# Optimization experiments

Hardware: AMD Instinct MI355X
Metric: run time of the kernel (lower is better)

The kernel has to match this reference:

```python
import jax, jax.numpy as jnp
import numpy as np
from jax import lax

BATCH = 32; SEQ_LEN = 336; ENC_IN = 7; MARK_IN = 4
D_MODEL = 512; D_FF = 2048; N_HEADS = 8; DK = 64; DV = 64
E_LAYERS = 3; D_BOTTLE = 128; PRED_LEN = 96
WINDOW = (4, 4, 4); INNER = 5


def _mask_sizes():
    # Pyraformer get_mask: True = masked out
    all_size = [SEQ_LEN]
    for w in WINDOW:
        all_size.append(all_size[-1] // w)
    S = sum(all_size)
    m = np.zeros((S, S), bool)  # True = may attend
    iw = INNER // 2
    starts = np.cumsum([0] + all_size)
    for l, sz in enumerate(all_size):
        st = int(starts[l])
        for i in range(st, st + sz):
            m[i, max(i - iw, st):min(i + iw + 1, st + sz)] = True
    for l in range(1, len(all_size)):
        st = int(starts[l])
        for i in range(st, st + all_size[l]):
            left = (st - all_size[l - 1]) + (i - st) * WINDOW[l - 1]
            right = st if i == st + all_size[l] - 1 else (st - all_size[l - 1]) + (i - st + 1) * WINDOW[l - 1]
            m[i, left:right] = True
            m[left:right, i] = True
    return ~m, all_size


def _refer_points(all_size):
    idx = np.zeros((all_size[0], len(all_size)), np.int64)
    for i in range(all_size[0]):
        idx[i, 0] = i
        former = i
        for j in range(1, len(all_size)):
            start = sum(all_size[:j])
            inner = former - (start - all_size[j - 1])
            former = start + min(inner // WINDOW[j - 1], all_size[j] - 1)
            idx[i, j] = former
    return idx


def _pos_enc(L, d):
    pos = np.arange(L)[:, None].astype(np.float32)
    div = np.exp(np.arange(0, d, 2).astype(np.float32) * (-np.log(10000.0) / d))
    pe = np.zeros((L, d), np.float32)
    pe[:, 0::2] = np.sin(pos * div)
    pe[:, 1::2] = np.cos(pos * div)
    return pe


def _ln(x, g, b, eps=1e-5):
    mu = jnp.mean(x, -1, keepdims=True)
    v = jnp.mean((x - mu) ** 2, -1, keepdims=True)
    return (x - mu) * lax.rsqrt(v + eps) * g + b


def setup_inputs():
    key = jax.random.key(0)
    ks = iter(jax.random.split(key, 64))
    def nrm(shape, s=0.02):
        return jax.random.normal(next(ks), shape, jnp.float32) * s
    mask, all_size = _mask_sizes()
    inp = {
        "x_enc": jax.random.normal(next(ks), (BATCH, SEQ_LEN, ENC_IN), jnp.float32),
        "x_mark_enc": jax.random.normal(next(ks), (BATCH, SEQ_LEN, MARK_IN), jnp.float32),
        "x_dec": jax.random.normal(next(ks), (BATCH, PRED_LEN, ENC_IN), jnp.float32),
        "x_mark_dec": jax.random.normal(next(ks), (BATCH, PRED_LEN, MARK_IN), jnp.float32),
        "conv_embed_w": nrm((D_MODEL, ENC_IN, 3), 0.1),
        "time_w": nrm((MARK_IN, D_MODEL)),
        "time_b": jnp.zeros((D_MODEL,), jnp.float32),
        "down_w": nrm((D_MODEL, D_BOTTLE)),
        "down_b": jnp.zeros((D_BOTTLE,), jnp.float32),
        "cscm_conv_w": nrm((3, D_BOTTLE, D_BOTTLE, 4), 0.05),
        "cscm_conv_b": jnp.zeros((3, D_BOTTLE), jnp.float32),
        "bn_g": jnp.ones((3, D_BOTTLE), jnp.float32),
        "bn_b": jnp.zeros((3, D_BOTTLE), jnp.float32),
        "up_w": nrm((D_BOTTLE, D_MODEL)),
        "up_b": jnp.zeros((D_MODEL,), jnp.float32),
        "cscm_ln_g": jnp.ones((D_MODEL,), jnp.float32),
        "cscm_ln_b": jnp.zeros((D_MODEL,), jnp.float32),
        "wq": nrm((E_LAYERS, D_MODEL, N_HEADS * DK)),
        "wk": nrm((E_LAYERS, D_MODEL, N_HEADS * DK)),
        "wv": nrm((E_LAYERS, D_MODEL, N_HEADS * DV)),
        "wo": nrm((E_LAYERS, N_HEADS * DV, D_MODEL)),
        "ln1_g": jnp.ones((E_LAYERS, D_MODEL), jnp.float32),
        "ln1_b": jnp.zeros((E_LAYERS, D_MODEL), jnp.float32),
        "ffn_w1": nrm((E_LAYERS, D_MODEL, D_FF)),
        "ffn_b1": jnp.zeros((E_LAYERS, D_FF), jnp.float32),
        "ffn_w2": nrm((E_LAYERS, D_FF, D_MODEL)),
        "ffn_b2": jnp.zeros((E_LAYERS, D_MODEL), jnp.float32),
        "ln2_g": jnp.ones((E_LAYERS, D_MODEL), jnp.float32),
        "ln2_b": jnp.zeros((E_LAYERS, D_MODEL), jnp.float32),
        "pred_w": nrm((len(all_size) * D_MODEL, PRED_LEN * ENC_IN)),
        "attn_mask": jnp.asarray(mask),                 # [S,S] bool, True = masked
        "indexes": jnp.asarray(_refer_points(all_size)),  # [336, 4] int64
    }
    return inp


def _forward(x_enc, x_mark_enc, conv_embed_w, time_w, time_b, down_w, down_b,
             cscm_conv_w, cscm_conv_b, bn_g, bn_b, up_w, up_b, cscm_ln_g, cscm_ln_b,
             wq, wk, wv, wo, ln1_g, ln1_b, ffn_w1, ffn_b1, ffn_w2, ffn_b2, ln2_g, ln2_b,
             pred_w, attn_mask, indexes):
    B = x_enc.shape[0]
    dn = ('NWC', 'OIW', 'NWC')
    # DataEmbedding: circular conv1d token embedding + sinusoidal pos + linear time-feature embedding
    xp = jnp.concatenate([x_enc[:, -1:], x_enc, x_enc[:, :1]], axis=1)  # circular pad, k=3
    tok = lax.conv_general_dilated(xp, conv_embed_w, (1,), 'VALID', dimension_numbers=dn)
    pe = jnp.asarray(_pos_enc(SEQ_LEN, D_MODEL))
    emb = tok + pe[None] + x_mark_enc @ time_w + time_b  # [B,336,512]
    # Bottleneck_Construct (CSCM): down-proj, strided convs per scale, up-proj, concat, LN
    x = emb @ down_w + down_b  # [B,336,128]
    outs = []
    for i in range(len(WINDOW)):
        x = lax.conv_general_dilated(x, cscm_conv_w[i], (WINDOW[i],), 'VALID', dimension_numbers=dn) + cscm_conv_b[i]
        x = x * bn_g[i] + bn_b[i]  # eval-mode BatchNorm1d (running mean 0 / var 1)
        x = jax.nn.elu(x)
        outs.append(x)  # lengths 84, 21, 5
    coarse = jnp.concatenate(outs, axis=1) @ up_w + up_b  # [B,110,512]
    seq = _ln(jnp.concatenate([emb, coarse], axis=1), cscm_ln_g, cscm_ln_b)  # [B,446,512]
    S = seq.shape[1]
    neg = jnp.where(attn_mask, jnp.float32(-1e9), jnp.float32(0.0))  # [S,S]
    scale = 1.0 / np.sqrt(DK).astype(np.float32)
    for l in range(E_LAYERS):  # post-norm encoder layers
        q = (seq @ wq[l]).reshape(B, S, N_HEADS, DK)
        k = (seq @ wk[l]).reshape(B, S, N_HEADS, DK)
        v = (seq @ wv[l]).reshape(B, S, N_HEADS, DV)
        attn = jax.nn.softmax(jnp.einsum('bihd,bjhd->bhij', q, k) * scale + neg, axis=-1)
        o = jnp.einsum('bhij,bjhd->bihd', attn, v).reshape(B, S, N_HEADS * DV)
        seq = _ln(seq + o @ wo[l], ln1_g[l], ln1_b[l])
        h = jax.nn.gelu(seq @ ffn_w1[l] + ffn_b1[l], approximate=False)
        seq = _ln(seq + h @ ffn_w2[l] + ffn_b2[l], ln2_g[l], ln2_b[l])
    # pyramidal readout: gather each scale's ancestor node for every fine position
    g = seq[:, indexes.reshape(-1), :].reshape(B, SEQ_LEN, -1)  # [B,336,4*512]
    enc_out = g[:, -1, :]  # [B,2048]
    return (enc_out @ pred_w).reshape(B, PRED_LEN, ENC_IN)


def reference(x_enc, x_mark_enc, x_dec, x_mark_dec, conv_embed_w, time_w, time_b,
              down_w, down_b, cscm_conv_w, cscm_conv_b, bn_g, bn_b, up_w, up_b,
              cscm_ln_g, cscm_ln_b, wq, wk, wv, wo, ln1_g, ln1_b, ffn_w1, ffn_b1,
              ffn_w2, ffn_b2, ln2_g, ln2_b, pred_w, attn_mask, indexes):
    # x_dec / x_mark_dec are unused by Pyraformer's forward (kept for signature parity)
    return _forward(x_enc, x_mark_enc, conv_embed_w, time_w, time_b, down_w, down_b,
                    cscm_conv_w, cscm_conv_b, bn_g, bn_b, up_w, up_b, cscm_ln_g, cscm_ln_b,
                    wq, wk, wv, wo, ln1_g, ln1_b, ffn_w1, ffn_b1, ffn_w2, ffn_b2,
                    ln2_g, ln2_b, pred_w, attn_mask, indexes)
```

## Files before the change

kernel.cpp:

```cpp
#include <hip/hip_runtime.h>
#include <math.h>

constexpr int BB   = 32;
constexpr int L    = 336;
constexpr int CIN  = 7;
constexpr int MARK = 4;
constexpr int D    = 512;
constexpr int DFF  = 2048;
constexpr int NH   = 8;
constexpr int HD   = 64;
constexpr int S    = 446;
constexpr int DBOT = 128;
constexpr int L1 = 84, L2 = 21, L3 = 5;
constexpr int LC = 110;
constexpr int NLAYER = 3;
constexpr int PRED_N = 672;
constexpr int MP   = 14336;
constexpr int NMAX = 12;
constexpr int MCONV1 = BB * L1;
constexpr int MCONV2P = 768;
constexpr int MCAT  = 3584;

using short8  = __attribute__((ext_vector_type(8))) short;
using float4v = __attribute__((ext_vector_type(4))) float;

struct SetsData {
    int nbr[S][NMAX];
    int idx[4][S];
    int cnt[4];
};

constexpr SetsData compute_sets() {
    SetsData sd{};
    constexpr int sizes[4]  = {336, 84, 21, 5};
    constexpr int starts[4] = {0, 336, 420, 441};
    for (int i = 0; i < S; ++i) {
        int li = 0, pi = i;
        if (i < 336)      { li = 0; pi = i; }
        else if (i < 420) { li = 1; pi = i - 336; }
        else if (i < 441) { li = 2; pi = i - 420; }
        else              { li = 3; pi = i - 441; }
        int cnt = 0;
        for (int d = -2; d <= 2; ++d) {
// ... 36 lines not shown

constexpr size_t psk_elems() {
    size_t mx = 4 * (size_t)BB * L * DBOT;
    {
        size_t v = 4 * (size_t)MCONV1 * DBOT; if (v > mx) mx = v;
        v = 4 * (size_t)MCONV2P * DBOT;       if (v > mx) mx = v;
    }
    for (int l = 0; l < NLAYER; ++l) {
        size_t Mc = (size_t)HS.cnt[l + 1] * 32;
        size_t Mpad = ((Mc + 127) / 128) * 128;
        { size_t v = 4 * Mpad * 512;  if (v > mx) mx = v; }
        if (Mc <= 512) { size_t v = 4 * Mpad * 2048; if (v > mx) mx = v; }
        size_t ks = (Mc <= 512) ? 8 : 4;
        size_t v = ks * Mpad * 512; if (v > mx) mx = v;
    }
    return mx;
}

__device__ inline short f2bf(float f) {
    union { float f; unsigned u; } v; v.f = f;
    unsigned r = v.u + 0x7fffu + ((v.u >> 16) & 1u);
    return (short)(r >> 16);
}
__device__ inline float bf2f(short h) {
    union { unsigned u; float f; } v; v.u = ((unsigned)(unsigned short)h) << 16;
    return v.f;
}

__device__ inline void gload_lds16(const void* g, void* l) {
    __builtin_amdgcn_global_load_lds(
        (const __attribute__((address_space(1))) void*)g,
        (__attribute__((address_space(3))) void*)l, 16, 0, 0);
}


template<int EPI>
__launch_bounds__(256, 4)
__global__ void mfma_gemm(const short* __restrict__ A, const short* __restrict__ Bt,
                          const float* __restrict__ bias, const float* __restrict__ bias2,
                          void* __restrict__ Cout, int Kd, int Nd,
                          int alvl, int clvl, int cnt,
                          const float* __restrict__ peT, short* __restrict__ Cout2) {
    __shared__ short As[2][128 * 32];
    __shared__ short Bs[2][128 * 32];
    int tid = threadIdx.x;
    int nwg  = gridDim.x * gridDim.y;
    int orig = blockIdx.y * gridDim.x + blockIdx.x;
    int qq = nwg >> 3, rr = nwg & 7;
    int xcd = orig & 7, idx = orig >> 3;
    int wgid = (xcd < rr ? xcd * (qq + 1) : rr * (qq + 1) + (xcd - rr) * qq) + idx;
    int m0 = (wgid / gridDim.x) * 128, n0 = (wgid % gridDim.x) * 128;

    int lane = tid & 63, wid = tid >> 6;
    int wm = wid >> 1, wn = wid & 1;
    int lr = lane & 15, lk = lane >> 4;

    size_t abase[2], bbase[2];
#pragma unroll
    for (int r = 0; r < 2; ++r) {
        int u = r * 256 + tid;
        int row = ((u >> 3) << 1) | ((u >> 2) & 1);
        int kg  = (u & 3) ^ ((u >> 3) & 3);
        int rm = m0 + row, ga;
        if (alvl >= 0) { int j = rm >> 5; if (j > cnt - 1) j = cnt - 1; ga = (rm & 31) * S + d_sets.idx[alvl][j]; }
        else ga = rm;
        abase[r] = (size_t)ga * Kd + kg * 8;
// ... 266 lines not shown
        __builtin_amdgcn_s_barrier();
    }

#pragma unroll
    for (int mi = 0; mi < 4; ++mi) {
        int gmc = m0 + wm * 64 + mi * 16 + lk * 4;
#pragma unroll
        for (int ni = 0; ni < 4; ++ni) {
            int gn = n0 + wn * 64 + ni * 16 + lr;
#pragma unroll
            for (int e = 0; e < 4; ++e)
                part[((size_t)kz * Mpad + gmc + e) * Nd + gn] = acc[mi][ni][e];
        }
    }
}

template<int EPI>
__launch_bounds__(256)
__global__ void reduce_sk(const float* __restrict__ part, const float* __restrict__ bias,
                          const float* __restrict__ bias2, short* __restrict__ Cout,
                          int Mpad, int Nd, int KS) {
    int idx = blockIdx.x * 256 + threadIdx.x;
    if (idx >= Mpad * Nd) return;
    float s = 0.0f;
    for (int k = 0; k < KS; ++k)
        s += part[(size_t)k * Mpad * Nd + idx];
    int n = idx % Nd;
    if (EPI == 3 || EPI == 4) s += bias[n];
    if (EPI == 3) s = 0.5f * s * (1.0f + erff(s * 0.70710678118654752f));
    if (EPI == 5) { s = s * bias[n] + bias2[n]; s = s > 0.0f ? s : (expf(s) - 1.0f); }
    Cout[idx] = f2bf(s);
}

__device__ inline void wtrans_tile(const float* __restrict__ W, short* __restrict__ Wt,
                                   int Kd, int Nd, int n0, int k0, int tid) {
    __shared__ float tile[32][33];
    int tx = tid & 31, ty = tid >> 5;
#pragma unroll
    for (int r = 0; r < 32; r += 8)
        tile[ty + r][tx] = W[(size_t)(k0 + ty + r) * Nd + n0 + tx];
    __syncthreads();
#pragma unroll
    for (int r = 0; r < 32; r += 8)
        Wt[(size_t)(n0 + ty + r) * Kd + k0 + tx] = f2bf(tile[tx][ty + r]);
}

constexpr int PE_N  = L * D;
constexpr int WE_N  = D * 32;
constexpr int XIM_N = BB * L * 32;
constexpr int MISC_N = PE_N + WE_N + XIM_N;
constexpr int PREP_BLKS = 3072 + 6144 + 640 + (MISC_N + 255) / 256;

__launch_bounds__(256)
__global__ void prep_all(const float* __restrict__ wq, const float* __restrict__ wk,
                         const float* __restrict__ wv, const float* __restrict__ wo,
                         short* __restrict__ wqkvT, short* __restrict__ woT,
                         const float* __restrict__ w1, const float* __restrict__ w2,
                         short* __restrict__ w1T, short* __restrict__ w2T,
                         const float* __restrict__ down_w, short* __restrict__ downT,
                         const float* __restrict__ up_w, short* __restrict__ upT,
                         const float* __restrict__ cw, const float* __restrict__ cb,
                         const float* __restrict__ bg, const float* __restrict__ bb,
                         short* __restrict__ cscmT, float* __restrict__ sc,
                         float* __restrict__ sh,
                         const float* __restrict__ x_enc, const float* __restrict__ x_mark,
                         const float* __restrict__ cew, const float* __restrict__ tw,
                         const float* __restrict__ tb, float* __restrict__ pe,
                         short* __restrict__ wE, short* __restrict__ xim) {
    int blk = blockIdx.x;
    int tid = threadIdx.x;
    if (blk < 3072) {
        int z = blk >> 8, rem = blk & 255;
        int l = z >> 2, part = z & 3;
        const float* src = (part == 0 ? wq : part == 1 ? wk : part == 2 ? wv : wo)
                           + (size_t)l * D * D;
        short* dst = (part < 3) ? wqkvT + (size_t)l * 3 * D * D + (size_t)part * D * D
                                : woT + (size_t)l * D * D;
        wtrans_tile(src, dst, D, D, (rem & 15) * 32, (rem >> 4) * 32, tid);
        return;
    }
    blk -= 3072;
    if (blk < 6144) {
        int z = blk >> 10, rem = blk & 1023;
        int l = z >> 1, part = z & 1;
        int bx = rem & 63, by = rem >> 6;
        int nt = part ? by : bx;
        int kt = part ? bx : by;
        if (part == 0)
            wtrans_tile(w1 + (size_t)l * D * DFF, w1T + (size_t)l * DFF * D,
                        D, DFF, nt * 32, kt * 32, tid);
        else
            wtrans_tile(w2 + (size_t)l * DFF * D, w2T + (size_t)l * D * DFF,
                        DFF, D, nt * 32, kt * 32, tid);
        return;
    }
    blk -= 6144;
    if (blk < 640) {
        if (blk < 64) {
            wtrans_tile(down_w, downT, D, DBOT, (blk & 3) * 32, (blk >> 2) * 32, tid);
        } else if (blk < 128) {
            int b2 = blk - 64;
            wtrans_tile(up_w, upT, DBOT, D, (b2 & 15) * 32, (b2 >> 4) * 32, tid);
        } else {
            int idx = (blk - 128) * 256 + tid;
            if (idx < 2 * DBOT * 512) {
                int l = idx >> 16;
                int rem = idx & 65535;
                int oc = rem >> 9, j = rem & 511;
                int r = j >> 7, c = j & 127;
                cscmT[idx] = f2bf(cw[(((size_t)l * DBOT + oc) * DBOT + c) * 4 + r]);
            }
            if (idx < 3 * DBOT) {
                sc[idx] = bg[idx];
                sh[idx] = cb[idx] * bg[idx] + bb[idx];
            }
        }
        return;
    }
    blk -= 640;
    {
        int idx = blk * 256 + tid;
        if (idx < PE_N) {
            int d = idx % D, t = idx / D;
            int e = d & ~1;
            float div = expf(-(float)e * (logf(10000.0f) / (float)D));
            float arg = (float)t * div;
            pe[idx] = (d & 1) ? cosf(arg) : sinf(arg);
            return;
        }
        int i2 = idx - PE_N;
        if (i2 < WE_N) {
            int k = i2 & 31, d = i2 >> 5;
            float v = 0.0f;
            if (k < 21) {
                int w = k / 7, i = k % 7;
// ... 70 lines not shown
#pragma unroll
    for (int jj = 0; jj < NMAX; ++jj) {
        float s = -1e30f;
        if (nb[jj] >= 0) {
            const short8 kv = *(const short8*)(QKV + (size_t)(b * S + nb[jj]) * 1536 + 512 + lane * 8);
            s = 0.0f;
#pragma unroll
            for (int e = 0; e < 8; ++e) s += qf[e] * bf2f(kv[e]);
            s += __shfl_xor(s, 1); s += __shfl_xor(s, 2); s += __shfl_xor(s, 4);
            s *= 0.125f;
        }
        sc[jj] = s;
    }
    float mx = sc[0];
#pragma unroll
    for (int jj = 1; jj < NMAX; ++jj) mx = fmaxf(mx, sc[jj]);
    float sum = 0.0f;
    float accv[8] = {};
#pragma unroll
    for (int jj = 0; jj < NMAX; ++jj) {
        float p = expf(sc[jj] - mx);
        sum += p;
        if (nb[jj] >= 0) {
            const short8 vv = *(const short8*)(QKV + (size_t)(b * S + nb[jj]) * 1536 + 1024 + lane * 8);
#pragma unroll
            for (int e = 0; e < 8; ++e) accv[e] += p * bf2f(vv[e]);
        }
    }
    float inv = 1.0f / sum;
    short8 ov;
#pragma unroll
    for (int e = 0; e < 8; ++e) ov[e] = f2bf(accv[e] * inv);
    *(short8*)(Ob + (size_t)wid * D + lane * 8) = ov;
}

__device__ inline float blk_reduce(float v, float* ws4, int tid) {
#pragma unroll
    for (int o = 32; o; o >>= 1) v += __shfl_xor(v, o);
    if ((tid & 63) == 0) ws4[tid >> 6] = v;
    __syncthreads();
    return ws4[0] + ws4[1] + ws4[2] + ws4[3];
}

__launch_bounds__(256)
__global__ void concat_ln_idx(const short* __restrict__ emb_bf, const float* __restrict__ coarse,
                              const float* __restrict__ g, const float* __restrict__ bta,
                              float* __restrict__ seq, short* __restrict__ seq_bf) {
    int row = blockIdx.x;
    int b = row & 31, j = row >> 5;
    int s = d_sets.idx[0][j];
    int orig = b * S + s;
    __shared__ float wsA[4];
    __shared__ float wsB[4];
    int tid = threadIdx.x;
    float x0, x1;
    if (s < L) {
        const short* src = emb_bf + ((size_t)b * L + s) * D;
        x0 = bf2f(src[tid]); x1 = bf2f(src[tid + 256]);
    } else {
        const float* src = coarse + ((size_t)b * LC + (s - L)) * D;
        x0 = src[tid]; x1 = src[tid + 256];
    }
    float mu = blk_reduce(x0 + x1, wsA, tid) * (1.0f / D);
    float d0 = x0 - mu, d1 = x1 - mu;
    float var = blk_reduce(d0 * d0 + d1 * d1, wsB, tid) * (1.0f / D);
    float rstd = rsqrtf(var + 1e-5f);
    float v0 = d0 * rstd * g[tid]       + bta[tid];
    float v1 = d1 * rstd * g[tid + 256] + bta[tid + 256];
    float* dst = seq + (size_t)orig * D;
    dst[tid] = v0; dst[tid + 256] = v1;
    short* dbf = seq_bf + (size_t)orig * D;
    dbf[tid] = f2bf(v0); dbf[tid + 256] = f2bf(v1);
}

// ... 34 lines not shown
                            float* __restrict__ part) {
    __shared__ float es[32][257];
    __shared__ float wsm[256][8];
    int tid = threadIdx.x;
    int n0 = blockIdx.x * 8;
    int ks = blockIdx.y;
    int k0 = ks * 256;
    const int pos[4] = {335, 419, 440, 445};
    int seg = ks >> 1;
    int dbase = (ks & 1) * 256;
#pragma unroll 8
    for (int r = 0; r < 32; ++r)
        es[r][tid] = seq[((size_t)r * S + pos[seg]) * D + dbase + tid];
#pragma unroll
    for (int e = 0; e < 8; ++e)
        wsm[tid][e] = w[(size_t)(k0 + tid) * PRED_N + n0 + e];
    __syncthreads();
    int b = tid >> 3, nn = tid & 7;
    float acc = 0.0f;
#pragma unroll 8
    for (int kk = 0; kk < 256; ++kk)
        acc += es[b][kk] * wsm[kk][nn];
    part[(size_t)ks * (BB * PRED_N) + (size_t)b * PRED_N + n0 + nn] = acc;
}

__launch_bounds__(256)
__global__ void pred_reduce_kernel(const float* __restrict__ part, float* __restrict__ out) {
    int idx = blockIdx.x * 256 + threadIdx.x;
    if (idx >= BB * PRED_N) return;
    float s = 0.0f;
#pragma unroll
    for (int k = 0; k < 8; ++k) s += part[(size_t)k * (BB * PRED_N) + idx];
    out[idx] = s;
}

extern "C" void kernel_launch(void* const* d_in, const int* in_sizes, int n_in,
                              void* d_out, int out_size, void* d_ws, size_t ws_size,
                              hipStream_t stream) {
    const float* x_enc      = (const float*)d_in[0];
    const float* x_mark_enc = (const float*)d_in[1];
    const float* conv_embed_w = (const float*)d_in[4];
    const float* time_w  = (const float*)d_in[5];
    const float* time_b  = (const float*)d_in[6];
    const float* down_w  = (const float*)d_in[7];
    const float* down_b  = (const float*)d_in[8];
    const float* cscm_w  = (const float*)d_in[9];
    const float* cscm_b  = (const float*)d_in[10];
    const float* bn_g    = (const float*)d_in[11];
    const float* bn_b    = (const float*)d_in[12];
    const float* up_w    = (const float*)d_in[13];
    const float* up_b    = (const float*)d_in[14];
    const float* cln_g   = (const float*)d_in[15];
    const float* cln_b   = (const float*)d_in[16];
    const float* wq      = (const float*)d_in[17];
    const float* wk      = (const float*)d_in[18];
    const float* wv      = (const float*)d_in[19];
    const float* wo      = (const float*)d_in[20];
    const float* ln1_g   = (const float*)d_in[21];
    const float* ln1_b   = (const float*)d_in[22];
    const float* ffn_w1  = (const float*)d_in[23];
    const float* ffn_b1  = (const float*)d_in[24];
    const float* ffn_w2  = (const float*)d_in[25];
    const float* ffn_b2  = (const float*)d_in[26];
    const float* ln2_g   = (const float*)d_in[27];
    const float* ln2_b   = (const float*)d_in[28];
    const float* pred_w  = (const float*)d_in[29];
    float* out = (float*)d_out;

    char* w8 = (char*)d_ws;
    size_t off = 0;
    auto alloc = [&](size_t bytes) {
        void* p = w8 + off;
        off = (off + bytes + 255) & ~(size_t)255;
        return p;
    };
    short* emb_bf = (short*)alloc((size_t)BB * L * D * 2);
    float* pe     = (float*)alloc((size_t)L * D * 4);
    short* xim    = (short*)alloc((size_t)BB * L * 32 * 2);
    short* wE     = (short*)alloc((size_t)D * 32 * 2);
    short* xd_bf  = (short*)alloc((size_t)BB * L * DBOT * 2);
    short* cs1_bf = (short*)alloc((size_t)MCONV2P * 512 * 2);
    short* cs2_bf = (short*)alloc((size_t)MCONV2P * DBOT * 2);
    short* cs3_bf = (short*)alloc((size_t)BB * L3 * DBOT * 2);
    float* coarse = (float*)alloc((size_t)MCAT * D * 4);
    float* seq    = (float*)alloc((size_t)BB * S * D * 4);
    float* part   = (float*)alloc((size_t)8 * BB * PRED_N * 4);
    float* partsk = (float*)alloc(psk_elems() * 4);
    short* seq_bf = (short*)alloc((size_t)MP * D * 2);
    short* QKV    = (short*)alloc((size_t)MP * 3 * D * 2);
    short* Ob     = (short*)alloc((size_t)MP * D * 2);
    short* hidden = QKV;
    short* wqkvT  = (short*)alloc((size_t)NLAYER * 3 * D * D * 2);
    short* woT    = (short*)alloc((size_t)NLAYER * D * D * 2);
    short* w1T    = (short*)alloc((size_t)NLAYER * DFF * D * 2);
    short* w2T    = (short*)alloc((size_t)NLAYER * D * DFF * 2);
    short* downT  = (short*)alloc((size_t)DBOT * D * 2);
    short* upT    = (short*)alloc((size_t)D * DBOT * 2);
    short* cscmT  = (short*)alloc((size_t)2 * DBOT * 512 * 2);
    float* csc_sc = (float*)alloc((size_t)3 * DBOT * 4);
    float* csc_sh = (float*)alloc((size_t)3 * DBOT * 4);
    (void)ws_size; (void)in_sizes; (void)n_in; (void)out_size;

    const int rowsL = BB * L;
    dim3 blk(256);

    prep_all<<<dim3(PREP_BLKS), blk, 0, stream>>>(
        wq, wk, wv, wo, wqkvT, woT,
        ffn_w1, ffn_w2, w1T, w2T,
        down_w, downT, up_w, upT,
        cscm_w, cscm_b, bn_g, bn_b, cscmT, csc_sc, csc_sh,
        x_enc, x_mark_enc, conv_embed_w, time_w, time_b, pe, wE, xim);
    mfma_gemm<6><<<dim3(D / 128, rowsL / 128), blk, 0, stream>>>(
        xim, wE, nullptr, nullptr, nullptr, 32, D, -1, -1, 0, pe, emb_bf);
    mfma_gemm_sk<<<dim3(1, rowsL / 128, 4), blk, 0, stream>>>(
        emb_bf, downT, partsk, D, DBOT, -1, 0);
    reduce_sk<4><<<dim3((rowsL * DBOT + 255) / 256), blk, 0, stream>>>(
        partsk, down_b, nullptr, xd_bf, rowsL, DBOT, 4);
    mfma_gemm_sk<<<dim3(1, MCONV1 / 128, 4), blk, 0, stream>>>(
        xd_bf, cscmT, partsk, 512, DBOT, -1, 0);
    reduce_sk<5><<<dim3((MCONV1 * DBOT + 255) / 256), blk, 0, stream>>>(
        partsk, csc_sc, csc_sh, cs1_bf, MCONV1, DBOT, 4);
    mfma_gemm_sk<<<dim3(1, MCONV2P / 128, 4), blk, 0, stream>>>(
        cs1_bf, cscmT + (size_t)DBOT * 512, partsk, 512, DBOT, -1, 0);
    reduce_sk<5><<<dim3((MCONV2P * DBOT + 255) / 256), blk, 0, stream>>>(
        partsk, csc_sc + DBOT, csc_sh + DBOT, cs2_bf, MCONV2P, DBOT, 4);
    cscm_conv_bf16<<<dim3(BB * L3), dim3(DBOT), 0, stream>>>(
        cs2_bf, L2, cs3_bf, cscm_w + 2 * DBOT * DBOT * 4,
        cscm_b + 2 * DBOT, bn_g + 2 * DBOT, bn_b + 2 * DBOT, L3);
    mfma_gemm_up<<<dim3(D / 128, MCAT / 128), blk, 0, stream>>>(
        cs1_bf, cs2_bf, cs3_bf, upT, up_b, coarse);
    concat_ln_idx<<<dim3(HS.cnt[0] * 32), blk, 0, stream>>>(
        emb_bf, coarse, cln_g, cln_b, seq, seq_bf);

    for (int l = 0; l < NLAYER; ++l) {
        const int inLvl = l, outLvl = l + 1;
        const int inCnt  = HS.cnt[l];
        const int outCnt = HS.cnt[l + 1];
        const int Mc   = outCnt * 32;
// ... 35 lines not shown
```

Baseline: 328.6 us.

## Fuse entire forward pass into one persistent cooperative kernel with grid syncs

Replaces the chain of separate kernel launches (prep, embedding GEMM, CSCM convs, per-layer QKV/attention/out-proj/FFN, LayerNorms, prediction) with a single persistent cooperative kernel. Stages run as virtual-block loops separated by grid.sync. Split-K reductions are folded into the add+LayerNorm row stages, and down/conv GEMMs now run without split-K. This removes launch overhead and inter-kernel gaps, but every stage boundary becomes a grid-wide barrier and small stages leave most blocks idle. It falls back to the old multi-kernel path if the cooperative launch fails.

Result: slower. 1.193 ms (+262.9%).

```diff
diff --git a/kernel.cpp b/kernel.cpp
--- a/kernel.cpp
+++ b/kernel.cpp
@@ -1,5 +1,8 @@
 #include <hip/hip_runtime.h>
+#include <hip/hip_cooperative_groups.h>
 #include <math.h>
+
+namespace cg = cooperative_groups;
 
 constexpr int BB   = 32;
 constexpr int L    = 336;
@@ -7,8 +10,6 @@
 constexpr int MARK = 4;
 constexpr int D    = 512;
 constexpr int DFF  = 2048;
-constexpr int NH   = 8;
-constexpr int HD   = 64;
 constexpr int S    = 446;
 constexpr int DBOT = 128;
 constexpr int L1 = 84, L2 = 21, L3 = 5;
@@ -111,6 +112,20 @@
         (const __attribute__((address_space(1))) void*)g,
         (__attribute__((address_space(3))) void*)l, 16, 0, 0);
 }
+
+__device__ inline float blk_reduce(float v, float* ws4, int tid) {
+#pragma unroll
+    for (int o = 32; o; o >>= 1) v += __shfl_xor(v, o);
+    if ((tid & 63) == 0) ws4[tid >> 6] = v;
+    __syncthreads();
+    return ws4[0] + ws4[1] + ws4[2] + ws4[3];
+}
+
+constexpr int PE_N  = L * D;
+constexpr int WE_N  = D * 32;
+constexpr int XIM_N = BB * L * 32;
+constexpr int MISC_N = PE_N + WE_N + XIM_N;
+constexpr int PREP_BLKS = 3072 + 6144 + 640 + (MISC_N + 255) / 256;
 
 
 template<int EPI>
@@ -443,8 +458,8 @@
     Cout[idx] = f2bf(s);
 }
 
-__device__ inline void wtrans_tile(const float* __restrict__ W, short* __restrict__ Wt,
-                                   int Kd, int Nd, int n0, int k0, int tid) {
+__device__ inline void wtrans_tile_s(const float* __restrict__ W, short* __restrict__ Wt,
+                                     int Kd, int Nd, int n0, int k0, int tid) {
     __shared__ float tile[32][33];
     int tx = tid & 31, ty = tid >> 5;
 #pragma unroll
@@ -455,12 +470,6 @@
     for (int r = 0; r < 32; r += 8)
         Wt[(size_t)(n0 + ty + r) * Kd + k0 + tx] = f2bf(tile[tx][ty + r]);
 }
-
-constexpr int PE_N  = L * D;
-constexpr int WE_N  = D * 32;
-constexpr int XIM_N = BB * L * 32;
-constexpr int MISC_N = PE_N + WE_N + XIM_N;
-constexpr int PREP_BLKS = 3072 + 6144 + 640 + (MISC_N + 255) / 256;
 
 __launch_bounds__(256)
 __global__ void prep_all(const float* __restrict__ wq, const float* __restrict__ wk,
@@ -487,7 +496,7 @@
                            + (size_t)l * D * D;
         short* dst = (part < 3) ? wqkvT + (size_t)l * 3 * D * D + (size_t)part * D * D
                                 : woT + (size_t)l * D * D;
-        wtrans_tile(src, dst, D, D, (rem & 15) * 32, (rem >> 4) * 32, tid);
+        wtrans_tile_s(src, dst, D, D, (rem & 15) * 32, (rem >> 4) * 32, tid);
         return;
     }
     blk -= 3072;
@@ -498,20 +507,20 @@
         int nt = part ? by : bx;
         int kt = part ? bx : by;
         if (part == 0)
-            wtrans_tile(w1 + (size_t)l * D * DFF, w1T + (size_t)l * DFF * D,
-                        D, DFF, nt * 32, kt * 32, tid);
+            wtrans_tile_s(w1 + (size_t)l * D * DFF, w1T + (size_t)l * DFF * D,
+                          D, DFF, nt * 32, kt * 32, tid);
         else
-            wtrans_tile(w2 + (size_t)l * DFF * D, w2T + (size_t)l * D * DFF,
-                        DFF, D, nt * 32, kt * 32, tid);
+            wtrans_tile_s(w2 + (size_t)l * DFF * D, w2T + (size_t)l * D * DFF,
+                          DFF, D, nt * 32, kt * 32, tid);
         return;
     }
     blk -= 6144;
     if (blk < 640) {
         if (blk < 64) {
-            wtrans_tile(down_w, downT, D, DBOT, (blk & 3) * 32, (blk >> 2) * 32, tid);
+            wtrans_tile_s(down_w, downT, D, DBOT, (blk & 3) * 32, (blk >> 2) * 32, tid);
         } else if (blk < 128) {
             int b2 = blk - 64;
-            wtrans_tile(up_w, upT, DBOT, D, (b2 & 15) * 32, (b2 >> 4) * 32, tid);
+            wtrans_tile_s(up_w, upT, DBOT, D, (b2 & 15) * 32, (b2 >> 4) * 32, tid);
         } else {
             int idx = (blk - 128) * 256 + tid;
             if (idx < 2 * DBOT * 512) {
@@ -648,14 +657,6 @@
 #pragma unroll
     for (int e = 0; e < 8; ++e) ov[e] = f2bf(accv[e] * inv);
     *(short8*)(Ob + (size_t)wid * D + lane * 8) = ov;
-}
-
-__device__ inline float blk_reduce(float v, float* ws4, int tid) {
-#pragma unroll
-    for (int o = 32; o; o >>= 1) v += __shfl_xor(v, o);
-    if ((tid & 63) == 0) ws4[tid >> 6] = v;
-    __syncthreads();
-    return ws4[0] + ws4[1] + ws4[2] + ws4[3];
 }
 
 __launch_bounds__(256)
@@ -756,6 +757,505 @@
 #pragma unroll
     for (int k = 0; k < 8; ++k) s += part[(size_t)k * (BB * PRED_N) + idx];
     out[idx] = s;
+}
+
+
+struct P {
+    const float *x_enc, *x_mark, *cew, *tw, *tb;
+    const float *down_w, *down_b, *cscm_w, *cscm_b, *bn_g, *bn_b;
+    const float *up_w, *up_b, *cln_g, *cln_b;
+    const float *wq, *wk, *wv, *wo, *ln1_g, *ln1_b;
+    const float *w1, *b1, *w2, *b2, *ln2_g, *ln2_b, *pred_w;
+    float* out;
+    short *emb_bf, *xim, *wE, *xd_bf, *cs1, *cs2, *cs3;
+    short *seq_bf, *QKV, *Ob;
+    short *wqkvT, *woT, *w1T, *w2T, *downT, *upT, *cscmT;
+    float *pe, *coarse, *seq, *part, *partsk, *csc_sc, *csc_sh;
+};
+
+__device__ inline void wtrans_tile_p(const float* __restrict__ W, short* __restrict__ Wt,
+                                     int Kd, int Nd, int n0, int k0, int tid,
+                                     float (*tile)[33]) {
+    int tx = tid & 31, ty = tid >> 5;
+#pragma unroll
+    for (int r = 0; r < 32; r += 8)
+        tile[ty + r][tx] = W[(size_t)(k0 + ty + r) * Nd + n0 + tx];
+    __syncthreads();
+#pragma unroll
+    for (int r = 0; r < 32; r += 8)
+        Wt[(size_t)(n0 + ty + r) * Kd + k0 + tx] = f2bf(tile[tx][ty + r]);
+}
+
+__device__ inline void prep_vb(const P& p, int blk, int tid, float (*tile)[33]) {
+    if (blk < 3072) {
+        int z = blk >> 8, rem = blk & 255;
+        int l = z >> 2, part = z & 3;
+        const float* src = (part == 0 ? p.wq : part == 1 ? p.wk : part == 2 ? p.wv : p.wo)
+                           + (size_t)l * D * D;
+        short* dst = (part < 3) ? p.wqkvT + (size_t)l * 3 * D * D + (size_t)part * D * D
+                                : p.woT + (size_t)l * D * D;
+        wtrans_tile_p(src, dst, D, D, (rem & 15) * 32, (rem >> 4) * 32, tid, tile);
+    } else if (blk < 3072 + 6144) {
+        int b2 = blk - 3072;
+        int z = b2 >> 10, rem = b2 & 1023;
+        int l = z >> 1, part = z & 1;
+        int bx = rem & 63, by = rem >> 6;
+        int nt = part ? by : bx;
+        int kt = part ? bx : by;
+        if (part == 0)
+            wtrans_tile_p(p.w1 + (size_t)l * D * DFF, p.w1T + (size_t)l * DFF * D,
+                          D, DFF, nt * 32, kt * 32, tid, tile);
+        else
+            wtrans_tile_p(p.w2 + (size_t)l * DFF * D, p.w2T + (size_t)l * D * DFF,
+                          DFF, D, nt * 32, kt * 32, tid, tile);
+    } else if (blk < 3072 + 6144 + 640) {
+        int b3 = blk - (3072 + 6144);
+        if (b3 < 64) {
+            wtrans_tile_p(p.down_w, p.downT, D, DBOT, (b3 & 3) * 32, (b3 >> 2) * 32, tid, tile);
+        } else if (b3 < 128) {
+            int b4 = b3 - 64;
+            wtrans_tile_p(p.up_w, p.upT, DBOT, D, (b4 & 15) * 32, (b4 >> 4) * 32, tid, tile);
+        } else {
+            int idx = (b3 - 128) * 256 + tid;
+            if (idx < 2 * DBOT * 512) {
+                int l = idx >> 16;
+                int rem = idx & 65535;
+                int oc = rem >> 9, j = rem & 511;
+                int r = j >> 7, c = j & 127;
+                p.cscmT[idx] = f2bf(p.cscm_w[(((size_t)l * DBOT + oc) * DBOT + c) * 4 + r]);
+            }
+            if (idx < 3 * DBOT) {
+                p.csc_sc[idx] = p.bn_g[idx];
+                p.csc_sh[idx] = p.cscm_b[idx] * p.bn_g[idx] + p.bn_b[idx];
+            }
+        }
+    } else {
+        int idx = (blk - (3072 + 6144 + 640)) * 256 + tid;
+        if (idx < PE_N) {
+            int d = idx % D, t = idx / D;
+            int e = d & ~1;
+            float div = expf(-(float)e * (logf(10000.0f) / (float)D));
+            float arg = (float)t * div;
+            p.pe[idx] = (d & 1) ? cosf(arg) : sinf(arg);
+        } else if (idx - PE_N < WE_N) {
+            int i2 = idx - PE_N;
+            int k = i2 & 31, d = i2 >> 5;
+            float v = 0.0f;
+            if (k < 21) {
+                int w = k / 7, i = k % 7;
+                v = p.cew[(size_t)d * (CIN * 3) + i * 3 + w];
+            } else if (k < 25) {
+                v = p.tw[(size_t)(k - 21) * D + d];
+            } else if (k == 25) {
+                v = p.tb[d];
+            }
+            p.wE[i2] = f2bf(v);
+        } else if (idx - PE_N - WE_N < XIM_N) {
+            int i3 = idx - PE_N - WE_N;
+            int k = i3 & 31, m = i3 >> 5;
+            int t = m % L, b = m / L;
+            float v = 0.0f;
+            if (k < 21) {
+                int w = k / 7, i = k % 7;
+                int s = t + w - 1;
+                if (s < 0) s = L - 1;
+                if (s >= L) s = 0;
+                v = p.x_enc[((size_t)b * L + s) * CIN + i];
+            } else if (k < 25) {
+                v = p.x_mark[(size_t)m * MARK + (k - 21)];
+            } else if (k == 25) {
+                v = 1.0f;
+            }
+            p.xim[i3] = f2bf(v);
+        }
+    }
+}
+
+__device__ __forceinline__ void gemm_tile(
+    const P& p, const short* __restrict__ A, const short* __restrict__ Bt,
+    short* As, short* Bs,
+    int Kd, int Nd, int m0, int n0, int kbase, int kb,
+    int amode, int alvl, int acnt, int clvl, int ccnt, int epi,
+    const float* __restrict__ bias, const float* __restrict__ bias2,
+    float* __restrict__ outF, short* __restrict__ outB, size_t outOff, int tid)
+{
+    int lane = tid & 63, wid = tid >> 6;
+    int wm = wid >> 1, wn = wid & 1;
+    int lr = lane & 15, lk = lane >> 4;
+
+    const short* aad[2];
+    size_t bbase[2];
+#pragma unroll
+    for (int r = 0; r < 2; ++r) {
+        int u = r * 256 + tid;
+        int row = ((u >> 3) << 1) | ((u >> 2) & 1);
+        int kg  = (u & 3) ^ ((u >> 3) & 3);
+        int rm = m0 + row;
+        const short* ab;
+        if (amode == 1) {
+            int j = rm >> 5; if (j > acnt - 1) j = acnt - 1;
+            ab = A + (size_t)((rm & 31) * S + d_sets.idx[alvl][j]) * Kd;
+        } else if (amode == 2) {
+            if (rm < BB * LC) {
+                int b = rm / LC, t = rm % LC;
+                if (t < L1)           ab = p.cs1 + (size_t)(b * L1 + t) * DBOT;
+                else if (t < L1 + L2) ab = p.cs2 + (size_t)(b * L2 + (t - L1)) * DBOT;
+                else                  ab = p.cs3 + (size_t)(b * L3 + (t - L1 - L2)) * DBOT;
+            } else ab = p.cs1;
+        } else {
+            ab = A + (size_t)rm * Kd;
+        }
+        aad[r] = ab + kbase + kg * 8;
+        bbase[r] = (size_t)(n0 + row) * Kd + kbase + kg * 8;
+    }
+    auto rd_off = [&](int row_) {
+        int rh = row_ >> 1;
+        int sx = lk ^ (rh & 3);
+        return (size_t)(rh * 8 + (row_ & 1) * 4 + sx) * 8;
+    };
+
+    float4v acc[4][4];
+#pragma unroll
+    for (int i = 0; i < 4; ++i)
+#pragma unroll
+        for (int j = 0; j < 4; ++j) acc[i][j] = 0;
+
+    const int nt = kb >> 5;
+#pragma unroll
+    for (int r = 0; r < 2; ++r) {
+        gload_lds16(aad[r], As + (size_t)(r * 256 + wid * 64) * 8);
+        gload_lds16(Bt + bbase[r], Bs + (size_t)(r * 256 + wid * 64) * 8);
+    }
+    for (int t = 0; t < nt; ++t) {
+        int cur = t & 1;
+        if (t + 1 < nt) {
+            int k0 = (t + 1) * 32;
+            int nb = (cur ^ 1) * 4096;
+#pragma unroll
+            for (int r = 0; r < 2; ++r) {
+                gload_lds16(aad[r] + k0, As + nb + (size_t)(r * 256 + wid * 64) * 8);
+                gload_lds16(Bt + bbase[r] + k0, Bs + nb + (size_t)(r * 256 + wid * 64) * 8);
+            }
+            asm volatile("s_waitcnt vmcnt(4)" ::: "memory");
+        } else {
+            asm volatile("s_waitcnt vmcnt(0)" ::: "memory");
+        }
+        __builtin_amdgcn_s_barrier();
+        short8 af[4], bfv[4];
+#pragma unroll
+        for (int mi = 0; mi < 4; ++mi)
+            af[mi] = *(const short8*)(As + cur * 4096 + rd_off(wm * 64 + mi * 16 + lr));
+#pragma unroll
+        for (int ni = 0; ni < 4; ++ni)
+            bfv[ni] = *(const short8*)(Bs + cur * 4096 + rd_off(wn * 64 + ni * 16 + lr));
+        __builtin_amdgcn_s_setprio(1);
+#pragma unroll
+        for (int mi = 0; mi < 4; ++mi)
+#pragma unroll
+            for (int ni = 0; ni < 4; ++ni)
+                acc[mi][ni] = __builtin_amdgcn_mfma_f32_16x16x32_bf16(
+                    af[mi], bfv[ni], acc[mi][ni], 0, 0, 0);
+        __builtin_amdgcn_s_setprio(0);
+        __builtin_amdgcn_s_barrier();
+    }
+
+#pragma unroll
+    for (int mi = 0; mi < 4; ++mi) {
+        int gmc = m0 + wm * 64 + mi * 16 + lk * 4;
+#pragma unroll
+        for (int ni = 0; ni < 4; ++ni) {
+            int gn = n0 + wn * 64 + ni * 16 + lr;
+            float bsv = (epi == 1 || epi == 3 || epi == 4) ? bias[gn] : 0.0f;
+            float sc = (epi == 5) ? bias[gn]  : 0.0f;
+            float sh = (epi == 5) ? bias2[gn] : 0.0f;
+#pragma unroll
+            for (int e = 0; e < 4; ++e) {
+                int rm = gmc + e, grow;
+                if (clvl >= 0) { int j = rm >> 5; if (j > ccnt - 1) j = ccnt - 1; grow = (rm & 31) * S + d_sets.idx[clvl][j]; }
+                else grow = rm;
+                float v = acc[mi][ni][e] + bsv;
+                if (epi == 3) v = 0.5f * v * (1.0f + erff(v * 0.70710678118654752f));
+                if (epi == 5) { v = v * sc + sh; v = v > 0.0f ? v : (expf(v) - 1.0f); }
+                if (epi == 6) {
+                    v += p.pe[(size_t)(grow % L) * D + gn];
+                    outB[(size_t)grow * Nd + gn] = f2bf(v);
+                } else if (epi == 1) {
+                    outF[(size_t)grow * Nd + gn] = v;
+                } else if (epi == 7) {
+                    outF[outOff + (size_t)grow * Nd + gn] = v;
+                } else {
+                    outB[(size_t)grow * Nd + gn] = f2bf(v);
+                }
+            }
+        }
+    }
+}
+
+__device__ inline void concat_ln_row(const P& p, int row, int tid, float* wsA, float* wsB) {
+    int b = row & 31, j = row >> 5;
+    int s = d_sets.idx[0][j];
+    int orig = b * S + s;
+    float x0, x1;
+    if (s < L) {
+        const short* src = p.emb_bf + ((size_t)b * L + s) * D;
+        x0 = bf2f(src[tid]); x1 = bf2f(src[tid + 256]);
+    } else {
+        const float* src = p.coarse + ((size_t)b * LC + (s - L)) * D;
+        x0 = src[tid]; x1 = src[tid + 256];
+    }
+    float mu = blk_reduce(x0 + x1, wsA, tid) * (1.0f / D);
+    float d0 = x0 - mu, d1 = x1 - mu;
+    float var = blk_reduce(d0 * d0 + d1 * d1, wsB, tid) * (1.0f / D);
+    float rstd = rsqrtf(var + 1e-5f);
+    float v0 = d0 * rstd * p.cln_g[tid]       + p.cln_b[tid];
+    float v1 = d1 * rstd * p.cln_g[tid + 256] + p.cln_b[tid + 256];
+    float* dst = p.seq + (size_t)orig * D;
+    dst[tid] = v0; dst[tid + 256] = v1;
+    short* dbf = p.seq_bf + (size_t)orig * D;
+    dbf[tid] = f2bf(v0); dbf[tid + 256] = f2bf(v1);
+}
+
+__device__ inline void add_ln_row(const P& p, int row, int tid, const float* bias,
+                                  const float* g, const float* bta,
+                                  int lvl, int Mpad, int KS, float* wsA, float* wsB) {
+    int b = row & 31, j = row >> 5;
+    int orig = b * S + d_sets.idx[lvl][j];
+    float a0 = 0.0f, a1 = 0.0f;
+    for (int k = 0; k < KS; ++k) {
+        const float* pr = p.partsk + ((size_t)k * Mpad + row) * D;
+        a0 += pr[tid];
+        a1 += pr[tid + 256];
+    }
+    if (bias) { a0 += bias[tid]; a1 += bias[tid + 256]; }
+    float* srow = p.seq + (size_t)orig * D;
+    float x0 = srow[tid] + a0;
+    float x1 = srow[tid + 256] + a1;
+    float mu = blk_reduce(x0 + x1, wsA, tid) * (1.0f / D);
+    float d0 = x0 - mu, d1 = x1 - mu;
+    float var = blk_reduce(d0 * d0 + d1 * d1, wsB, tid) * (1.0f / D);
+    float rstd = rsqrtf(var + 1e-5f);
+    float v0 = d0 * rstd * g[tid]       + bta[tid];
+    float v1 = d1 * rstd * g[tid + 256] + bta[tid + 256];
+    srow[tid] = v0; srow[tid + 256] = v1;
+    short* dbf = p.seq_bf + (size_t)orig * D;
+    dbf[tid] = f2bf(v0); dbf[tid + 256] = f2bf(v1);
+}
+
+__device__ inline void attn_vb(const P& p, int vb, int tid, int lvl, int cnt) {
+    int wid = vb * 4 + (tid >> 6);
+    if (wid >= cnt * 32) return;
+    int lane = tid & 63;
+    int b = wid & 31, j = wid >> 5;
+    int i = d_sets.idx[lvl][j];
+    const short8 qv = *(const short8*)(p.QKV + (size_t)(b * S + i) * 1536 + lane * 8);
+    float qf[8];
+#pragma unroll
+    for (int e = 0; e < 8; ++e) qf[e] = bf2f(qv[e]);
+    int nb[NMAX];
+#pragma unroll
+    for (int jj = 0; jj < NMAX; ++jj) nb[jj] = d_sets.nbr[i][jj];
+    float sc[NMAX];
+#pragma unroll
+    for (int jj = 0; jj < NMAX; ++jj) {
+        float s = -1e30f;
+        if (nb[jj] >= 0) {
+            const short8 kv = *(const short8*)(p.QKV + (size_t)(b * S + nb[jj]) * 1536 + 512 + lane * 8);
+            s = 0.0f;
+#pragma unroll
+            for (int e = 0; e < 8; ++e) s += qf[e] * bf2f(kv[e]);
+            s += __shfl_xor(s, 1); s += __shfl_xor(s, 2); s += __shfl_xor(s, 4);
+            s *= 0.125f;
+        }
+        sc[jj] = s;
+    }
+    float mx = sc[0];
+#pragma unroll
+    for (int jj = 1; jj < NMAX; ++jj) mx = fmaxf(mx, sc[jj]);
+    float sum = 0.0f;
+    float accv[8] = {};
+#pragma unroll
+    for (int jj = 0; jj < NMAX; ++jj) {
+        float pr = expf(sc[jj] - mx);
+        sum += pr;
+        if (nb[jj] >= 0) {
+            const short8 vv = *(const short8*)(p.QKV + (size_t)(b * S + nb[jj]) * 1536 + 1024 + lane * 8);
+#pragma unroll
+            for (int e = 0; e < 8; ++e) accv[e] += pr * bf2f(vv[e]);
+        }
+    }
+    float inv = 1.0f / sum;
+    short8 ov;
+#pragma unroll
+    for (int e = 0; e < 8; ++e) ov[e] = f2bf(accv[e] * inv);
+    *(short8*)(p.Ob + (size_t)wid * D + lane * 8) = ov;
+}
+
+__device__ inline void conv3_vb(const P& p, int vb, int tid, char* lds_pool) {
+    float* insh = (float*)lds_pool;
+    int half = tid >> 7, t2 = tid & 127;
+    int bid = vb * 2 + half;
+    int to = bid % L3, b = bid / L3;
+    float* my = insh + half * 512;
+#pragma unroll
+    for (int r = 0; r < 4; ++r)
+        my[r * DBOT + t2] = bf2f(p.cs2[((size_t)(b * L2 + to * 4 + r)) * DBOT + t2]);
+    __syncthreads();
+    const float* w = p.cscm_w + 2 * DBOT * DBOT * 4;
+    float acc = p.cscm_b[2 * DBOT + t2];
+    const float* wr = w + (size_t)t2 * (DBOT * 4);
+    for (int c = 0; c < DBOT; ++c) {
+#pragma unroll
+        for (int r = 0; r < 4; ++r)
+            acc += my[r * DBOT + c] * wr[c * 4 + r];
+    }
+    acc = acc * p.bn_g[2 * DBOT + t2] + p.bn_b[2 * DBOT + t2];
+    p.cs3[((size_t)(b * L3 + to)) * DBOT + t2] = f2bf(acc > 0.0f ? acc : (expf(acc) - 1.0f));
+    __syncthreads();
+}
+
+__device__ inline void pred_vb(const P& p, int vb, int tid, char* lds_pool) {
+    float (*es)[257] = (float(*)[257])lds_pool;
+    float (*wsm)[8]  = (float(*)[8])(lds_pool + 32 * 257 * 4);
+    int n0 = (vb % 84) * 8;
+    int ks = vb / 84;
+    int k0 = ks * 256;
+    const int pos[4] = {335, 419, 440, 445};
+    int seg = ks >> 1;
+    int dbase = (ks & 1) * 256;
+#pragma unroll 8
+    for (int r = 0; r < 32; ++r)
+        es[r][tid] = p.seq[((size_t)r * S + pos[seg]) * D + dbase + tid];
+#pragma unroll
+    for (int e = 0; e < 8; ++e)
+        wsm[tid][e] = p.pred_w[(size_t)(k0 + tid) * PRED_N + n0 + e];
+    __syncthreads();
+    int b = tid >> 3, nn = tid & 7;
+    float acc = 0.0f;
+#pragma unroll 8
+    for (int kk = 0; kk < 256; ++kk)
+        acc += es[b][kk] * wsm[kk][nn];
+    p.part[(size_t)ks * (BB * PRED_N) + (size_t)b * PRED_N + n0 + nn] = acc;
+    __syncthreads();
+}
+
+__launch_bounds__(256, 2)
+__global__ void fused_fwd(P p) {
+    __shared__ __align__(16) char lds_pool[41088];
+    __shared__ float wsA[4], wsB[4];
+    short* As = (short*)lds_pool;
+    short* Bs = (short*)(lds_pool + 16384);
+    cg::grid_group grid = cg::this_grid();
+    int tid = threadIdx.x;
+    int nbk = gridDim.x;
+
+    {
+        float (*tile)[33] = (float(*)[33])lds_pool;
+        for (int vb = blockIdx.x; vb < PREP_BLKS; vb += nbk) {
+            prep_vb(p, vb, tid, tile);
+            __syncthreads();
+        }
+    }
+    grid.sync();
+    for (int vb = blockIdx.x; vb < 4 * 84; vb += nbk) {
+        int bx = vb & 3, by = vb >> 2;
+        gemm_tile(p, p.xim, p.wE, As, Bs, 32, D, by * 128, bx * 128, 0, 32,
+                  0, 0, 0, -1, 0, 6, nullptr, nullptr, nullptr, p.emb_bf, 0, tid);
+    }
+    grid.sync();
+    for (int vb = blockIdx.x; vb < 84; vb += nbk)
+        gemm_tile(p, p.emb_bf, p.downT, As, Bs, 512, DBOT, vb * 128, 0, 0, 512,
+                  0, 0, 0, -1, 0, 4, p.down_b, nullptr, nullptr, p.xd_bf, 0, tid);
+    grid.sync();
+    for (int vb = blockIdx.x; vb < 21; vb += nbk)
+        gemm_tile(p, p.xd_bf, p.cscmT, As, Bs, 512, DBOT, vb * 128, 0, 0, 512,
+                  0, 0, 0, -1, 0, 5, p.csc_sc, p.csc_sh, nullptr, p.cs1, 0, tid);
+    grid.sync();
+    for (int vb = blockIdx.x; vb < 6; vb += nbk)
+        gemm_tile(p, p.cs1, p.cscmT + (size_t)DBOT * 512, As, Bs, 512, DBOT, vb * 128, 0, 0, 512,
+                  0, 0, 0, -1, 0, 5, p.csc_sc + DBOT, p.csc_sh + DBOT, nullptr, p.cs2, 0, tid);
+    grid.sync();
+    for (int vb = blockIdx.x; vb < 80; vb += nbk)
+        conv3_vb(p, vb, tid, lds_pool);
+    grid.sync();
+    for (int vb = blockIdx.x; vb < 4 * 28; vb += nbk) {
+        int bx = vb & 3, by = vb >> 2;
+        gemm_tile(p, p.cs1, p.upT, As, Bs, DBOT, D, by * 128, bx * 128, 0, DBOT,
+                  2, 0, 0, -1, 0, 1, p.up_b, nullptr, p.coarse, nullptr, 0, tid);
+    }
+    grid.sync();
+    {
+        int c0 = d_sets.cnt[0] * 32;
+        for (int vb = blockIdx.x; vb < c0; vb += nbk)
+            concat_ln_row(p, vb, tid, wsA, wsB);
+    }
+    grid.sync();
+
+    for (int l = 0; l < NLAYER; ++l) {
+        int inCnt = d_sets.cnt[l], outCnt = d_sets.cnt[l + 1];
+        int Mc = outCnt * 32;
+        int mtIn = (inCnt * 32 + 127) >> 7;
+        int Mpad = ((Mc + 127) >> 7) << 7;
+        int mtOut = Mpad >> 7;
+        int KS2 = (Mc <= 512) ? 8 : 4;
+        int kb2 = DFF / KS2;
+
+        for (int vb = blockIdx.x; vb < 12 * mtIn; vb += nbk) {
+            int bx = vb % 12, by = vb / 12;
+            gemm_tile(p, p.seq_bf, p.wqkvT + (size_t)l * 3 * D * D, As, Bs,
+                      512, 3 * D, by * 128, bx * 128, 0, 512,
+                      1, l, inCnt, l, inCnt, 2, nullptr, nullptr, nullptr, p.QKV, 0, tid);
+        }
+        grid.sync();
+        for (int vb = blockIdx.x; vb < outCnt * 8; vb += nbk)
+            attn_vb(p, vb, tid, l + 1, outCnt);
+        grid.sync();
+        for (int vb = blockIdx.x; vb < 4 * mtOut * 4; vb += nbk) {
+            int bx = vb & 3;
+            int rest = vb >> 2;
+            int by = rest % mtOut, kz = rest / mtOut;
+            gemm_tile(p, p.Ob, p.woT + (size_t)l * D * D, As, Bs,
+                      512, D, by * 128, bx * 128, kz * 128, 128,
+                      0, 0, 0, -1, 0, 7, nullptr, nullptr, p.partsk, nullptr,
+                      (size_t)kz * Mpad * D, tid);
+        }
+        grid.sync();
+        for (int vb = blockIdx.x; vb < Mc; vb += nbk)
+            add_ln_row(p, vb, tid, nullptr, p.ln1_g + (size_t)l * D, p.ln1_b + (size_t)l * D,
+                       l + 1, Mpad, 4, wsA, wsB);
+        grid.sync();
+        for (int vb = blockIdx.x; vb < 16 * mtOut; vb += nbk) {
+            int bx = vb % 16, by = vb / 16;
+            gemm_tile(p, p.seq_bf, p.w1T + (size_t)l * DFF * D, As, Bs,
+                      512, DFF, by * 128, bx * 128, 0, 512,
+                      1, l + 1, outCnt, -1, 0, 3, p.b1 + (size_t)l * DFF, nullptr,
+                      nullptr, p.QKV, 0, tid);
+        }
+        grid.sync();
+        for (int vb = blockIdx.x; vb < 4 * mtOut * KS2; vb += nbk) {
+            int bx = vb & 3;
+            int rest = vb >> 2;
+            int by = rest % mtOut, kz = rest / mtOut;
+            gemm_tile(p, p.QKV, p.w2T + (size_t)l * D * DFF, As, Bs,
+                      DFF, D, by * 128, bx * 128, kz * kb2, kb2,
+                      0, 0, 0, -1, 0, 7, nullptr, nullptr, p.partsk, nullptr,
+                      (size_t)kz * Mpad * D, tid);
+        }
+        grid.sync();
+        for (int vb = blockIdx.x; vb < Mc; vb += nbk)
+            add_ln_row(p, vb, tid, p.b2 + (size_t)l * D, p.ln2_g + (size_t)l * D,
+                       p.ln2_b + (size_t)l * D, l + 1, Mpad, KS2, wsA, wsB);
+        grid.sync();
+    }
+
+    for (int vb = blockIdx.x; vb < 672; vb += nbk)
+        pred_vb(p, vb, tid, lds_pool);
+    grid.sync();
+    for (int i = blockIdx.x * 256 + tid; i < BB * PRED_N; i += nbk * 256) {
+        float s = 0.0f;
+#pragma unroll
+        for (int k = 0; k < 8; ++k) s += p.part[(size_t)k * (BB * PRED_N) + i];
+        p.out[i] = s;
+    }
 }
 
 extern "C" void kernel_launch(void* const* d_in, const int* in_sizes, int n_in,
@@ -794,9 +1294,9 @@
     char* w8 = (char*)d_ws;
     size_t off = 0;
     auto alloc = [&](size_t bytes) {
-        void* p = w8 + off;
+        void* pp = w8 + off;
         off = (off + bytes + 255) & ~(size_t)255;
-        return p;
+        return pp;
     };
     short* emb_bf = (short*)alloc((size_t)BB * L * D * 2);
     float* pe     = (float*)alloc((size_t)L * D * 4);
@@ -828,6 +1328,39 @@
     const int rowsL = BB * L;
     dim3 blk(256);
 
+    P prm;
+    prm.x_enc = x_enc; prm.x_mark = x_mark_enc; prm.cew = conv_embed_w;
+    prm.tw = time_w; prm.tb = time_b;
+    prm.down_w = down_w; prm.down_b = down_b; prm.cscm_w = cscm_w; prm.cscm_b = cscm_b;
+    prm.bn_g = bn_g; prm.bn_b = bn_b; prm.up_w = up_w; prm.up_b = up_b;
+    prm.cln_g = cln_g; prm.cln_b = cln_b;
+    prm.wq = wq; prm.wk = wk; prm.wv = wv; prm.wo = wo;
+    prm.ln1_g = ln1_g; prm.ln1_b = ln1_b;
+    prm.w1 = ffn_w1; prm.b1 = ffn_b1; prm.w2 = ffn_w2; prm.b2 = ffn_b2;
+    prm.ln2_g = ln2_g; prm.ln2_b = ln2_b; prm.pred_w = pred_w; prm.out = out;
+    prm.emb_bf = emb_bf; prm.xim = xim; prm.wE = wE; prm.xd_bf = xd_bf;
+    prm.cs1 = cs1_bf; prm.cs2 = cs2_bf; prm.cs3 = cs3_bf;
+    prm.seq_bf = seq_bf; prm.QKV = QKV; prm.Ob = Ob;
+    prm.wqkvT = wqkvT; prm.woT = woT; prm.w1T = w1T; prm.w2T = w2T;
+    prm.downT = downT; prm.upT = upT; prm.cscmT = cscmT;
+    prm.pe = pe; prm.coarse = coarse; prm.seq = seq; prm.part = part;
+    prm.partsk = partsk; prm.csc_sc = csc_sc; prm.csc_sh = csc_sh;
+
+    bool coop_done = false;
+    int maxBlk = 0;
+    if (hipOccupancyMaxActiveBlocksPerMultiprocessor(
+            &maxBlk, reinterpret_cast<const void*>(&fused_fwd), 256, 0) == hipSuccess
+        && maxBlk > 0) {
+        if (maxBlk > 3) maxBlk = 3;
+        int grid = maxBlk * 256;
+        void* args[] = { &prm };
+        if (hipLaunchCooperativeKernel(reinterpret_cast<const void*>(&fused_fwd),
+                                       dim3(grid), dim3(256), args, 0, stream)
+            == hipSuccess)
+            coop_done = true;
+    }
+    if (coop_done) return;
+
     prep_all<<<dim3(PREP_BLKS), blk, 0, stream>>>(
         wq, wk, wv, wo, wqkvT, woT,
         ffn_w1, ffn_w2, w1T, w2T,
```
